# Optimization experiments

Measured on AMD Instinct MI355X. Metric: run time of the kernel, lower is better.

The kernel has to match this reference:

```python
import jax, jax.numpy as jnp
import numpy as np

FOCUS = 3.0
EPS = 1e-6


def setup_inputs() -> dict:
    key = jax.random.key(0)
    ks = jax.random.split(key, 8)
    C, h = 768, 12
    d = C // h
    H = W = T = 16
    l = 4
    Nx = H * W * T * l
    Nm = H * W * T
    B = 2

    def w(k, sh, s=0.02):
        return jax.random.normal(k, sh, jnp.float32) * s

    return {
        "x": jax.random.normal(ks[0], (Nx, B, C), jnp.float32),
        "memory": jax.random.normal(ks[1], (Nm, B, C), jnp.float32),
        "w_q": w(ks[2], (C, C)),
        "w_k": w(ks[3], (C, C)),
        "w_v": w(ks[4], (C, C)),
        "w_proj": w(ks[5], (C, C)),
        "b_proj": jnp.zeros((C,), jnp.float32),
        "dwc_w": w(ks[6], (d, 1, 5, 5)),
        "dwc_b": jnp.zeros((d,), jnp.float32),
        "scale": w(ks[7], (1, 1, C)),
        "H": H, "W": W, "T": T, "l": l,
    }


def _process(t, scale_sp):
    # focusing feature map: relu, rescale, elementwise power, renormalize to original norm
    t = jax.nn.relu(t) + EPS
    t = t / scale_sp
    n = jnp.linalg.norm(t, axis=-1, keepdims=True)
    tp = t ** FOCUS
    return tp / jnp.linalg.norm(tp, axis=-1, keepdims=True) * n


def _dwconv(v5, w, b):
    # depthwise conv2d, kernel 5, pad 2; v5: (B*h, d, H, W*T), w: (d,1,5,5)
    out = jax.lax.conv_general_dilated(
        v5, w, window_strides=(1, 1), padding=((2, 2), (2, 2)),
        dimension_numbers=("NCHW", "OIHW", "NCHW"),
        feature_group_count=v5.shape[1])
    return out + b[None, :, None, None]


def reference(x, memory, w_q, w_k, w_v, w_proj, b_proj, dwc_w, dwc_b, scale, H, W, T, l):
    x = x.transpose(1, 0, 2)          # (B, Nx, C)
    memory = memory.transpose(1, 0, 2)  # (B, Nm, C)
    B, Nx, C = x.shape
    Nm = memory.shape[1]
    d = dwc_w.shape[0]
    h = C // d

    q = jnp.einsum("bnc,dc->bnd", x, w_q)
    k = jnp.einsum("bnc,dc->bnd", memory, w_k)
    v = jnp.einsum("bnc,dc->bnd", memory, w_v)

    scale_sp = jax.nn.softplus(scale)
    q = _process(q, scale_sp)
    k = _process(k, scale_sp)

    q = q.reshape(B, Nx, h, d).transpose(0, 2, 1, 3)  # (B,h,Nx,d)
    k = k.reshape(B, Nm, h, d).transpose(0, 2, 1, 3)  # (B,h,Nm,d)
    v = v.reshape(B, Nm, h, d).transpose(0, 2, 1, 3)  # (B,h,Nm,d)

    k_mean = k.mean(axis=2, keepdims=True)            # (B,h,1,d)
    z = 1.0 / (jnp.einsum("bhnd,bhmd->bhnm", q, k_mean) + EPS)  # (B,h,Nx,1)

    inv = float(Nm) ** -0.5
    kv = jnp.einsum("bhnd,bhne->bhde", k * inv, v * inv)        # (B,h,d,d)
    out = jnp.einsum("bhnd,bhde->bhne", q, kv) * z              # (B,h,Nx,d)
    out = out.transpose(0, 2, 1, 3).reshape(B, Nx, C)

    # depthwise conv enhancement on v over (H, W*T) grid
    v5 = v.reshape(B * h, H, W, T, d).transpose(0, 4, 1, 2, 3).reshape(B * h, d, H, W * T)
    dwc = _dwconv(v5, dwc_w, dwc_b)                   # (B*h, d, H, W*T)
    dwc = dwc.reshape(B, C, Nm).transpose(0, 2, 1)    # (B, Nm, C)
    out = out + jnp.tile(dwc, (1, l, 1))              # (B, Nx, C)

    out = jnp.einsum("bnc,dc->bnd", out, w_proj) + b_proj
    return out.transpose(1, 0, 2)                     # (Nx, B, C)
```

## Files before the change

kernel.cpp:

```cpp
#include <hip/hip_runtime.h>

#define CD 768
#define NHEAD 12
#define DH 64
#define BSZ 2
#define NM_ 4096
#define NX_ 16384
#define EPSF 1e-6f
#define KSTR 1536
#define KVCH 32

using bf16x8 = __attribute__((ext_vector_type(8))) short;
using f32x4  = __attribute__((ext_vector_type(4))) float;

__device__ inline unsigned short bf16r(float f) {
  union { float f; unsigned u; } un; un.f = f;
  unsigned u = un.u;
  u += 0x7fffu + ((u >> 16) & 1u);
  return (unsigned short)(u >> 16);
}
__device__ inline float b2f(unsigned short u) {
  union { unsigned u; float f; } x; x.u = ((unsigned)u) << 16; return x.f;
}
__device__ inline float asf(unsigned u) {
  union { unsigned u; float f; } x; x.u = u; return x.f;
}
__device__ inline void gl2lds16(const void* g, void* l) {
  __builtin_amdgcn_global_load_lds(
      (const __attribute__((address_space(1))) void*)g,
      (__attribute__((address_space(3))) void*)l, 16, 0, 0);
}

__global__ __launch_bounds__(256) void prep_k(const float* __restrict__ w0, const float* __restrict__ w1,
                                              const float* __restrict__ w2, const float* __restrict__ w3,
                                              const float* __restrict__ scale,
                                              unsigned short* __restrict__ o0, unsigned short* __restrict__ o1,
                                              unsigned short* __restrict__ o2, unsigned short* __restrict__ o3,
                                              float* __restrict__ sp) {
  int bx = blockIdx.x;
  if (bx < 2304) {
    int m = bx / 576;
    int i = (bx % 576) * 256 + threadIdx.x;
    const float* w = m == 0 ? w0 : m == 1 ? w1 : m == 2 ? w2 : w3;
    unsigned short* o = m == 0 ? o0 : m == 1 ? o1 : m == 2 ? o2 : o3;
    float4 v = ((const float4*)w)[i];
    ushort4 u; u.x = bf16r(v.x); u.y = bf16r(v.y); u.z = bf16r(v.z); u.w = bf16r(v.w);
    ((ushort4*)o)[i] = u;
  } else {
    int i = (bx - 2304) * 256 + threadIdx.x;
    if (i < CD) sp[i] = log1pf(expf(scale[i]));
  }
}

__global__ __launch_bounds__(256) void cvt_k(const float* __restrict__ s,
                                             unsigned short* __restrict__ d, int n8) {
  int i = blockIdx.x * 256 + threadIdx.x;
  if (i >= n8) return;
  const float4* sp = (const float4*)s;
  float4 f0 = sp[(size_t)i * 2], f1 = sp[(size_t)i * 2 + 1];
  unsigned short u[8];
  u[0] = bf16r(f0.x); u[1] = bf16r(f0.y); u[2] = bf16r(f0.z); u[3] = bf16r(f0.w);
  u[4] = bf16r(f1.x); u[5] = bf16r(f1.y); u[6] = bf16r(f1.z); u[7] = bf16r(f1.w);
  *(int4*)(d + (size_t)i * 8) = *(int4*)u;
}

template<int OUTBF>
__global__ __launch_bounds__(256) void gemm128(const unsigned short* __restrict__ A,
                                               const unsigned short* __restrict__ B,
                                               void* __restrict__ Cv,
                                               const float* __restrict__ bias,
                                               int M, int N, int K) {
  __shared__ __align__(16) unsigned short As[128 * 32];
  __shared__ __align__(16) unsigned short Bs[128 * 32];
  const int m0 = blockIdx.x * 128, n0 = blockIdx.y * 128;
  const int tid = threadIdx.x, wave = tid >> 6, lane = tid & 63;
  const int quad = lane >> 4, l16 = lane & 15;
  const int wm = (wave >> 1) * 64, wn = (wave & 1) * 64;
  const int srow = lane >> 2, scol = (lane & 3) * 8;
  f32x4 acc[4][4] = {};
  for (int k0 = 0; k0 < K; k0 += 32) {
    __syncthreads();
    #pragma unroll
    for (int c2 = 0; c2 < 2; ++c2) {
      int ch = wave * 2 + c2;
      gl2lds16(A + (size_t)(m0 + ch * 16 + srow) * K + k0 + scol, (void*)(As + ch * 512));
      gl2lds16(B + (size_t)(n0 + ch * 16 + srow) * K + k0 + scol, (void*)(Bs + ch * 512));
    }
    __syncthreads();
    bf16x8 a[4], bb[4];
    #pragma unroll
    for (int t = 0; t < 4; ++t) {
      a[t]  = *(const bf16x8*)(As + (wm + t * 16 + l16) * 32 + quad * 8);
      bb[t] = *(const bf16x8*)(Bs + (wn + t * 16 + l16) * 32 + quad * 8);
    }
    #pragma unroll
    for (int tm = 0; tm < 4; ++tm)
      #pragma unroll
      for (int tn = 0; tn < 4; ++tn)
        acc[tm][tn] = __builtin_amdgcn_mfma_f32_16x16x32_bf16(a[tm], bb[tn], acc[tm][tn], 0, 0, 0);
  }
  #pragma unroll
  for (int tm = 0; tm < 4; ++tm)
    #pragma unroll
    for (int tn = 0; tn < 4; ++tn) {
      const int col = n0 + wn + tn * 16 + l16;
      const float bv = bias ? bias[col] : 0.f;
      #pragma unroll
      for (int r = 0; r < 4; ++r) {
        const int row = m0 + wm + tm * 16 + quad * 4 + r;
        float v = acc[tm][tn][r] + bv;
        if (OUTBF) ((unsigned short*)Cv)[(size_t)row * N + col] = bf16r(v);
        else       ((float*)Cv)[(size_t)row * N + col] = v;
      }
    }
}

template<int OUTBF>
__global__ __launch_bounds__(512, 2) void gemm256(const unsigned short* __restrict__ A,
                                                  const unsigned short* __restrict__ B,
                                                  void* __restrict__ Cv,
                                                  const float* __restrict__ bias,
                                                  int M, int N, int K) {
  __shared__ __align__(16) unsigned short As[4][256 * 32];
  __shared__ __align__(16) unsigned short Bs[4][256 * 32];
  const int m0 = blockIdx.x * 256, n0 = blockIdx.y * 256;
  const int tid = threadIdx.x, w = tid >> 6, lane = tid & 63;
  const int quad = lane >> 4, l16 = lane & 15;
  const int wm = (w >> 2) * 128, wn = (w & 3) * 64;
  const int NS = K >> 5;
  const int srow = 16 * w + (lane >> 2);
  const int c0 = lane & 3;
  const int scol = (c0 ^ ((srow >> 1) & 3)) * 8;
  const size_t arow = (size_t)(m0 + srow) * K;
  const size_t brow = (size_t)(n0 + srow) * K;
  const int fq = (quad ^ ((l16 >> 1) & 3)) * 8;

  auto stageA = [&](int s) {
    unsigned short* l = &As[s & 3][0] + w * 512;
    const size_t col = (size_t)s * 32 + scol;
    gl2lds16(A + arow + col, (void*)l);
    gl2lds16(A + arow + (size_t)128 * K + col, (void*)(l + 4096));
  };
  auto stageB = [&](int s) {
    unsigned short* l = &Bs[s & 3][0] + w * 512;
    const size_t col = (size_t)s * 32 + scol;
    gl2lds16(B + brow + col, (void*)l);
    gl2lds16(B + brow + (size_t)128 * K + col, (void*)(l + 4096));
  };

  f32x4 acc[8][4] = {};
  stageA(0); stageB(0);
  stageA(1); stageB(1);
  stageA(2); stageB(2);

  for (int s = 0; s < NS; ++s) {
    if (s < NS - 2)       asm volatile("s_waitcnt vmcnt(8)");
    else if (s == NS - 2) asm volatile("s_waitcnt vmcnt(4)");
    else                  asm volatile("s_waitcnt vmcnt(0)");
    __builtin_amdgcn_s_barrier();
    const unsigned short* sa = &As[s & 3][0];
    const unsigned short* sb = &Bs[s & 3][0];
    const bool st = (s + 3) < NS;
    bf16x8 av[4], bv[4];
    #pragma unroll
    for (int f = 0; f < 4; ++f) {
      av[f] = *(const bf16x8*)(sa + (wm + f * 16 + l16) * 32 + fq);
      bv[f] = *(const bf16x8*)(sb + (wn + f * 16 + l16) * 32 + fq);
    }
    if (st) stageA(s + 3);
    __builtin_amdgcn_s_setprio(1);
    #pragma unroll
    for (int mf = 0; mf < 4; ++mf)
      #pragma unroll
      for (int nf = 0; nf < 4; ++nf)
        acc[mf][nf] = __builtin_amdgcn_mfma_f32_16x16x32_bf16(av[mf], bv[nf], acc[mf][nf], 0, 0, 0);
    __builtin_amdgcn_s_setprio(0);
    __builtin_amdgcn_s_barrier();
    bf16x8 aw[4];
    #pragma unroll
    for (int f = 0; f < 4; ++f)
      aw[f] = *(const bf16x8*)(sa + (wm + 64 + f * 16 + l16) * 32 + fq);
    if (st) stageB(s + 3);
    __builtin_amdgcn_s_setprio(1);
    #pragma unroll
    for (int mf = 0; mf < 4; ++mf)
      #pragma unroll
      for (int nf = 0; nf < 4; ++nf)
        acc[4 + mf][nf] = __builtin_amdgcn_mfma_f32_16x16x32_bf16(aw[mf], bv[nf], acc[4 + mf][nf], 0, 0, 0);
    __builtin_amdgcn_s_setprio(0);
  }
  #pragma unroll
  for (int mf = 0; mf < 8; ++mf)
    #pragma unroll
    for (int nf = 0; nf < 4; ++nf) {
      const int col = n0 + wn + nf * 16 + l16;
      const float bvl = bias ? bias[col] : 0.f;
      #pragma unroll
      for (int r = 0; r < 4; ++r) {
        const int row = m0 + wm + mf * 16 + quad * 4 + r;
        float v = acc[mf][nf][r] + bvl;
        if (OUTBF) ((unsigned short*)Cv)[(size_t)row * N + col] = bf16r(v);
        else       ((float*)Cv)[(size_t)row * N + col] = v;
      }
    }
}

__global__ __launch_bounds__(256) void process_rows(float* __restrict__ X,
                                                    const float* __restrict__ sp) {
  const int row = blockIdx.x;
  const int tid = threadIdx.x;
  float* xr = X + (size_t)row * CD;
  float tv[3];
  float n2 = 0.f, m2 = 0.f;
  #pragma unroll
  for (int i = 0; i < 3; ++i) {
    int c = tid + i * 256;
    float t = fmaxf(xr[c], 0.f) + EPSF;
    t = t / sp[c];
    tv[i] = t;
    float t2 = t * t;
    n2 += t2;
    float p = t2 * t;
    m2 += p * p;
  }
  #pragma unroll
  for (int off = 32; off; off >>= 1) {
    n2 += __shfl_down(n2, off, 64);
    m2 += __shfl_down(m2, off, 64);
  }
  __shared__ float rn[4], rm[4];
  if ((tid & 63) == 0) { rn[tid >> 6] = n2; rm[tid >> 6] = m2; }
  __syncthreads();
  float N2 = rn[0] + rn[1] + rn[2] + rn[3];
  float M2 = rm[0] + rm[1] + rm[2] + rm[3];
  float factor = sqrtf(N2 / M2);
  unsigned short* xo = (unsigned short*)xr;
  #pragma unroll
  for (int i = 0; i < 3; ++i) {
    int c = tid + i * 256;
    float t = tv[i];
    xo[c] = bf16r(t * t * t * factor);
  }
}

__global__ __launch_bounds__(256) void kv_part_k(const unsigned short* __restrict__ Kp,
                                                 const unsigned short* __restrict__ Vp,
                                                 float* __restrict__ kvp,
                                                 float* __restrict__ kmp) {
  const int bh = blockIdx.x, chunk = blockIdx.y;
  const int b = bh / NHEAD, h = bh % NHEAD;
  const int n0 = chunk * 128;
  __shared__ __align__(16) unsigned short ks[128 * 72];
  __shared__ __align__(16) unsigned short vs[128 * 72];
  const int tid = threadIdx.x;
  #pragma unroll
  for (int it = 0; it < 4; ++it) {
    int g = it * 256 + tid;
    int row = g >> 3, c8 = (g & 7) * 8;
    int4 ka = *(const int4*)(Kp + ((size_t)(n0 + row) * BSZ + b) * KSTR + h * 64 + c8);
    int4 va = *(const int4*)(Vp + ((size_t)(n0 + row) * BSZ + b) * CD + h * 64 + c8);
    *(int4*)(ks + row * 72 + c8) = ka;
    *(int4*)(vs + row * 72 + c8) = va;
  }
  __syncthreads();
  const int d0 = (tid >> 4) * 4, e0 = (tid & 15) * 4;
  float acc[4][4] = {};
  #pragma unroll 4
  for (int n = 0; n < 128; ++n) {
    ushort4 kd = *(const ushort4*)(ks + n * 72 + d0);
    ushort4 ve = *(const ushort4*)(vs + n * 72 + e0);
    float kf[4] = {b2f(kd.x), b2f(kd.y), b2f(kd.z), b2f(kd.w)};
    float vf[4] = {b2f(ve.x), b2f(ve.y), b2f(ve.z), b2f(ve.w)};
    #pragma unroll
    for (int i = 0; i < 4; ++i)
      #pragma unroll
      for (int j = 0; j < 4; ++j) acc[i][j] += kf[i] * vf[j];
  }
  float* outp = kvp + ((size_t)chunk * 24 + bh) * 4096;
  #pragma unroll
  for (int i = 0; i < 4; ++i) {
    float4 o; o.x = acc[i][0]; o.y = acc[i][1]; o.z = acc[i][2]; o.w = acc[i][3];
    *(float4*)(outp + (d0 + i) * 64 + e0) = o;
  }
  if (tid < 64) {
    float s = 0.f;
    for (int n = 0; n < 128; ++n) s += b2f(ks[n * 72 + tid]);
    kmp[((size_t)chunk * 24 + bh) * 64 + tid] = s;
  }
}

__global__ __launch_bounds__(256) void kv_reduce_k(const float* __restrict__ kvp,
                                                   const float* __restrict__ kmp,
                                                   unsigned short* __restrict__ kvT,
                                                   float* __restrict__ km) {
  const int tid = threadIdx.x;
  const int bx = blockIdx.x;
  if (bx < 24) {
    __shared__ float t[64 * 65];
    float acc[16] = {};
    const float* base = kvp + (size_t)bx * 4096 + tid * 16;
    for (int c = 0; c < KVCH; ++c) {
      const float* p = base + (size_t)c * 24 * 4096;
      #pragma unroll
      for (int i = 0; i < 4; ++i) {
        float4 v = *(const float4*)(p + i * 4);
        acc[i * 4 + 0] += v.x; acc[i * 4 + 1] += v.y; acc[i * 4 + 2] += v.z; acc[i * 4 + 3] += v.w;
      }
    }
    const int d = tid >> 2, e0 = (tid & 3) * 16;
    #pragma unroll
    for (int i = 0; i < 16; ++i) t[d * 65 + e0 + i] = acc[i] * (1.f / NM_);
    __syncthreads();
    const int e = tid >> 2, dd0 = (tid & 3) * 16;
    ushort4 o[4];
    #pragma unroll
    for (int i = 0; i < 16; ++i)
      ((unsigned short*)o)[i] = bf16r(t[(dd0 + i) * 65 + e]);
    unsigned short* dst = kvT + (size_t)bx * 4096 + e * 64 + dd0;
    *(ushort4*)(dst) = o[0]; *(ushort4*)(dst + 4) = o[1];
    *(ushort4*)(dst + 8) = o[2]; *(ushort4*)(dst + 12) = o[3];
  } else {
    int i = (bx - 24) * 256 + tid;
    if (i < 24 * 64) {
      int bhh = i >> 6, d = i & 63;
      float s = 0.f;
      for (int c = 0; c < KVCH; ++c) s += kmp[((size_t)c * 24 + bhh) * 64 + d];
      int b = bhh / NHEAD, h = bhh % NHEAD;
      km[b * CD + h * 64 + d] = s * (1.f / NM_);
    }
  }
}

__global__ __launch_bounds__(256) void dwconv_k(const unsigned short* __restrict__ Vp,
                                                const float* __restrict__ w,
                                                const float* __restrict__ bias,
                                                unsigned short* __restrict__ outp) {
  __shared__ __align__(16) unsigned ls32[16 * 20 * 32];
  __shared__ float wsm[64 * 25];
  __shared__ float bsm[64];
  const int tid = threadIdx.x;
  const int bh = blockIdx.x, b = bh / NHEAD, h = bh % NHEAD;
  const int x0 = blockIdx.y * 16;
  for (int i = tid; i < 1600; i += 256) wsm[i] = w[i];
  if (tid < 64) bsm[tid] = bias[tid];
  const int lch = (tid & 7) * 8;
  #pragma unroll
  for (int it = 0; it < 10; ++it) {
    int p = it * 32 + (tid >> 3);
    int y = p / 20, xp = p % 20;
    int xx = x0 + xp - 2;
    int4 val = {0, 0, 0, 0};
    if (xx >= 0 && xx < 256)
      val = *(const int4*)(Vp + ((size_t)((y << 8) + xx) * BSZ + b) * CD + h * 64 + lch);
    *(int4*)((unsigned short*)ls32 + p * 64 + lch) = val;
  }
  __syncthreads();
  const int cp = tid & 31;
  const int xs = tid >> 5;
  float wr0[25], wr1[25];
  #pragma unroll
  for (int t = 0; t < 25; ++t) { wr0[t] = wsm[(cp * 2) * 25 + t]; wr1[t] = wsm[(cp * 2 + 1) * 25 + t]; }
  const float b0 = bsm[cp * 2], b1 = bsm[cp * 2 + 1];
  for (int y = 0; y < 16; ++y) {
    float a00 = b0, a01 = b1, a10 = b0, a11 = b1;
    #pragma unroll
    for (int dy = 0; dy < 5; ++dy) {
      int yy = y + dy - 2;
      if (yy < 0 || yy >= 16) continue;
      #pragma unroll
      for (int dx = 0; dx < 5; ++dx) {
        int base = (yy * 20 + xs * 2 + dx) * 32 + cp;
        unsigned u0 = ls32[base], u1 = ls32[base + 32];
        float w0 = wr0[dy * 5 + dx], w1 = wr1[dy * 5 + dx];
        a00 += w0 * asf(u0 << 16);  a01 += w1 * asf(u0 & 0xffff0000u);
        a10 += w0 * asf(u1 << 16);  a11 += w1 * asf(u1 & 0xffff0000u);
      }
    }
    const int x = x0 + xs * 2;
    size_t o = ((size_t)((y << 8) + x) * BSZ + b) * CD + h * 64 + cp * 2;
    ushort2 s0; s0.x = bf16r(a00); s0.y = bf16r(a01);
    ushort2 s1; s1.x = bf16r(a10); s1.y = bf16r(a11);
    *(ushort2*)(outp + o) = s0;
    *(ushort2*)(outp + o + (size_t)BSZ * CD) = s1;
  }
}

__global__ __launch_bounds__(256) void attn_mfma(const unsigned short* __restrict__ Qb,
                                                 const unsigned short* __restrict__ kvT,
                                                 const float* __restrict__ km,
                                                 const unsigned short* __restrict__ dwcb,
                                                 unsigned short* __restrict__ tmpb) {
  __shared__ __align__(16) unsigned short qs[128 * 64];
  __shared__ __align__(16) unsigned short kvs[64 * 64];
  __shared__ float kms[64];
  __shared__ float zs[128];
  const int bh = blockIdx.x, b = bh / NHEAD, h = bh % NHEAD;
  const int n0 = blockIdx.y * 128;
  const int tid = threadIdx.x, wave = tid >> 6, lane = tid & 63;
  const int quad = lane >> 4, l16 = lane & 15;
  #pragma unroll
  for (int c2 = 0; c2 < 4; ++c2) {
    int ch = wave * 4 + c2;
    int row = ch * 8 + (lane >> 3);
    int col = (lane & 7) * 8;
    gl2lds16(Qb + ((size_t)(n0 + row) * BSZ + b) * KSTR + h * 64 + col, (void*)(qs + ch * 512));
  }
  #pragma unroll
  for (int c2 = 0; c2 < 2; ++c2) {
    int ch = wave * 2 + c2;
    int e = ch * 8 + (lane >> 3);
    int col = (lane & 7) * 8;
    gl2lds16(kvT + (size_t)bh * 4096 + e * 64 + col, (void*)(kvs + ch * 512));
  }
  if (tid < 64) kms[tid] = km[b * CD + h * 64 + tid];
  __syncthreads();
  if (tid < 128) {
    float s = 0.f;
    for (int d2 = 0; d2 < 64; ++d2) s += b2f(qs[tid * 64 + d2]) * kms[d2];
    zs[tid] = 1.f / (s + EPSF);
  }
  __syncthreads();
  f32x4 acc[2][4] = {};
  #pragma unroll
  for (int kh = 0; kh < 2; ++kh) {
    bf16x8 a0 = *(const bf16x8*)(qs + (wave * 32 + l16) * 64 + kh * 32 + quad * 8);
    bf16x8 a1 = *(const bf16x8*)(qs + (wave * 32 + 16 + l16) * 64 + kh * 32 + quad * 8);
    bf16x8 bt[4];
    #pragma unroll
    for (int tn = 0; tn < 4; ++tn)
      bt[tn] = *(const bf16x8*)(kvs + (tn * 16 + l16) * 64 + kh * 32 + quad * 8);
    #pragma unroll
    for (int tn = 0; tn < 4; ++tn) {
      acc[0][tn] = __builtin_amdgcn_mfma_f32_16x16x32_bf16(a0, bt[tn], acc[0][tn], 0, 0, 0);
      acc[1][tn] = __builtin_amdgcn_mfma_f32_16x16x32_bf16(a1, bt[tn], acc[1][tn], 0, 0, 0);
    }
  }
  #pragma unroll
  for (int tm = 0; tm < 2; ++tm)
    #pragma unroll
    for (int tn = 0; tn < 4; ++tn)
      #pragma unroll
      for (int r = 0; r < 4; ++r) {
        int rl = wave * 32 + tm * 16 + quad * 4 + r;
        int n = n0 + rl;
        int m = n & (NM_ - 1);
        int c = h * 64 + tn * 16 + l16;
        float val = acc[tm][tn][r] * zs[rl] + b2f(dwcb[((size_t)m * BSZ + b) * CD + c]);
        tmpb[((size_t)n * BSZ + b) * CD + c] = bf16r(val);
      }
}

extern "C" void kernel_launch(void* const* d_in, const int* in_sizes, int n_in,
                              void* d_out, int out_size, void* d_ws, size_t ws_size,
                              hipStream_t stream) {
  const float* x      = (const float*)d_in[0];
  const float* memory = (const float*)d_in[1];
  const float* w_q    = (const float*)d_in[2];
  const float* w_k    = (const float*)d_in[3];
  const float* w_v    = (const float*)d_in[4];
  const float* w_proj = (const float*)d_in[5];
  const float* b_proj = (const float*)d_in[6];
  const float* dwc_w  = (const float*)d_in[7];
  const float* dwc_b  = (const float*)d_in[8];
  const float* scale  = (const float*)d_in[9];
  float* out = (float*)d_out;

  const int Mq = NX_ * BSZ;
  const int Mm = NM_ * BSZ;

  char* ws = (char*)d_ws;
  size_t off = 0;
  auto alloc = [&](size_t bytes) -> void* {
    void* p = ws + off;
    off += (bytes + 255) & ~(size_t)255;
    return p;
  };
  float* q    = (float*)alloc((size_t)Mq * CD * 4);
  float* kbuf = (float*)alloc((size_t)Mm * CD * 4);
  float* kvp  = (float*)alloc((size_t)KVCH * 24 * 4096 * 4);
  float* kmp  = (float*)alloc((size_t)KVCH * 24 * 64 * 4);
  float* km   = (float*)alloc((size_t)BSZ * CD * 4);
  float* sp   = (float*)alloc(CD * 4);
  unsigned short* tmpb = (unsigned short*)alloc((size_t)Mq * CD * 2);
  unsigned short* vb   = (unsigned short*)alloc((size_t)Mm * CD * 2);
  unsigned short* dwcb = (unsigned short*)alloc((size_t)Mm * CD * 2);
  unsigned short* kvT  = (unsigned short*)alloc((size_t)BSZ * NHEAD * DH * DH * 2);
  unsigned short* wqb  = (unsigned short*)alloc((size_t)CD * CD * 2);
  unsigned short* wkb  = (unsigned short*)alloc((size_t)CD * CD * 2);
  unsigned short* wvb  = (unsigned short*)alloc((size_t)CD * CD * 2);
  unsigned short* wpb  = (unsigned short*)alloc((size_t)CD * CD * 2);

  unsigned short* xb   = tmpb;
  unsigned short* memb = dwcb;

  prep_k<<<2307, 256, 0, stream>>>(w_q, w_k, w_v, w_proj, scale, wqb, wkb, wvb, wpb, sp);

  cvt_k<<<(Mq * CD / 8 + 255) / 256, 256, 0, stream>>>(x, xb, Mq * CD / 8);
  cvt_k<<<(Mm * CD / 8 + 255) / 256, 256, 0, stream>>>(memory, memb, Mm * CD / 8);

  gemm256<0><<<dim3(Mq / 256, CD / 256), 512, 0, stream>>>(xb,   wqb, q,    nullptr, Mq, CD, CD);
  gemm128<0><<<dim3(Mm / 128, CD / 128), 256, 0, stream>>>(memb, wkb, kbuf, nullptr, Mm, CD, CD);
  gemm128<1><<<dim3(Mm / 128, CD / 128), 256, 0, stream>>>(memb, wvb, vb,   nullptr, Mm, CD, CD);

  process_rows<<<Mq, 256, 0, stream>>>(q, sp);
  process_rows<<<Mm, 256, 0, stream>>>(kbuf, sp);

  const unsigned short* qb = (const unsigned short*)q;
  const unsigned short* kb = (const unsigned short*)kbuf;

  kv_part_k<<<dim3(24, KVCH), 256, 0, stream>>>(kb, vb, kvp, kmp);
  kv_reduce_k<<<30, 256, 0, stream>>>(kvp, kmp, kvT, km);

  dwconv_k<<<dim3(BSZ * NHEAD, 16), 256, 0, stream>>>(vb, dwc_w, dwc_b, dwcb);

  attn_mfma<<<dim3(BSZ * NHEAD, NX_ / 128), 256, 0, stream>>>(qb, kvT, km, dwcb, tmpb);

  gemm256<0><<<dim3(Mq / 256, CD / 256), 512, 0, stream>>>(tmpb, wpb, out, b_proj, Mq, CD, CD);
}
```

Measured before the change: 514.4 us.

## Replace 256x256 GEMM with 256x192-tile 1024-thread kernel using triple-buffered LDS

Replaces the 512-thread 256x256-tile GEMM used for the Q and output projections with a 1024-thread kernel using 256x192 tiles, giving a 128x4 grid instead of 128x3. Each of the 16 waves now owns a 64x48 sub-tile. The K loop is hardcoded to 768 and uses a three-buffer LDS ring, unrolled by three, with one barrier per step instead of two. The goal is more blocks and waves to fill the CUs and less synchronisation, at the cost of smaller per-wave tiles with lower MFMA reuse and a kernel that only works for K=768.

After: 510.5 us. About the same (-0.8%).

```diff
diff --git a/kernel.cpp b/kernel.cpp
--- a/kernel.cpp
+++ b/kernel.cpp
@@ -116,83 +116,72 @@
 }
 
 template<int OUTBF>
-__global__ __launch_bounds__(512, 2) void gemm256(const unsigned short* __restrict__ A,
-                                                  const unsigned short* __restrict__ B,
-                                                  void* __restrict__ Cv,
-                                                  const float* __restrict__ bias,
-                                                  int M, int N, int K) {
-  __shared__ __align__(16) unsigned short As[4][256 * 32];
-  __shared__ __align__(16) unsigned short Bs[4][256 * 32];
-  const int m0 = blockIdx.x * 256, n0 = blockIdx.y * 256;
+__global__ __launch_bounds__(1024, 4) void gemm256c(const unsigned short* __restrict__ A,
+                                                    const unsigned short* __restrict__ B,
+                                                    void* __restrict__ Cv,
+                                                    const float* __restrict__ bias,
+                                                    int M, int N) {
+  __shared__ __align__(16) unsigned short As0[8192], As1[8192], As2[8192];
+  __shared__ __align__(16) unsigned short Bs0[8192], Bs1[8192], Bs2[8192];
+  const int m0 = blockIdx.x * 256, n0 = blockIdx.y * 192;
   const int tid = threadIdx.x, w = tid >> 6, lane = tid & 63;
   const int quad = lane >> 4, l16 = lane & 15;
-  const int wm = (w >> 2) * 128, wn = (w & 3) * 64;
-  const int NS = K >> 5;
-  const int srow = 16 * w + (lane >> 2);
-  const int c0 = lane & 3;
-  const int scol = (c0 ^ ((srow >> 1) & 3)) * 8;
-  const size_t arow = (size_t)(m0 + srow) * K;
-  const size_t brow = (size_t)(n0 + srow) * K;
+  const int wm = (w >> 2) * 64, wn = (w & 3) * 48;
   const int fq = (quad ^ ((l16 >> 1) & 3)) * 8;
-
-  auto stageA = [&](int s) {
-    unsigned short* l = &As[s & 3][0] + w * 512;
-    const size_t col = (size_t)s * 32 + scol;
-    gl2lds16(A + arow + col, (void*)l);
-    gl2lds16(A + arow + (size_t)128 * K + col, (void*)(l + 4096));
+  const int lrow = lane >> 2, lc = lane & 3;
+  f32x4 acc[4][3] = {};
+
+  auto stage = [&](int s, unsigned short* la, unsigned short* lb) {
+    const int kc = s * 32;
+    #pragma unroll
+    for (int j = 0; j < 2; ++j) {
+      const int c = w * 2 + j;
+      if (c < 16) {
+        const int grow = c * 16 + lrow;
+        const int gcol = (lc ^ ((grow >> 1) & 3)) * 8;
+        gl2lds16(A + (size_t)(m0 + grow) * 768 + kc + gcol, (void*)(la + c * 512));
+      } else {
+        const int bc = (c < 28) ? c - 16 : c - 28;
+        const int grow = bc * 16 + lrow;
+        const int gcol = (lc ^ ((grow >> 1) & 3)) * 8;
+        gl2lds16(B + (size_t)(n0 + grow) * 768 + kc + gcol, (void*)(lb + (c - 16) * 512));
+      }
+    }
   };
-  auto stageB = [&](int s) {
-    unsigned short* l = &Bs[s & 3][0] + w * 512;
-    const size_t col = (size_t)s * 32 + scol;
-    gl2lds16(B + brow + col, (void*)l);
-    gl2lds16(B + brow + (size_t)128 * K + col, (void*)(l + 4096));
-  };
-
-  f32x4 acc[8][4] = {};
-  stageA(0); stageB(0);
-  stageA(1); stageB(1);
-  stageA(2); stageB(2);
-
-  for (int s = 0; s < NS; ++s) {
-    if (s < NS - 2)       asm volatile("s_waitcnt vmcnt(8)");
-    else if (s == NS - 2) asm volatile("s_waitcnt vmcnt(4)");
-    else                  asm volatile("s_waitcnt vmcnt(0)");
+
+  auto body = [&](int s, const unsigned short* sa, const unsigned short* sb,
+                  unsigned short* na, unsigned short* nb) {
+    if (s < 23) asm volatile("s_waitcnt vmcnt(2)");
+    else        asm volatile("s_waitcnt vmcnt(0)");
     __builtin_amdgcn_s_barrier();
-    const unsigned short* sa = &As[s & 3][0];
-    const unsigned short* sb = &Bs[s & 3][0];
-    const bool st = (s + 3) < NS;
-    bf16x8 av[4], bv[4];
-    #pragma unroll
-    for (int f = 0; f < 4; ++f) {
+    bf16x8 av[4], bv[3];
+    #pragma unroll
+    for (int f = 0; f < 4; ++f)
       av[f] = *(const bf16x8*)(sa + (wm + f * 16 + l16) * 32 + fq);
-      bv[f] = *(const bf16x8*)(sb + (wn + f * 16 + l16) * 32 + fq);
-    }
-    if (st) stageA(s + 3);
+    #pragma unroll
+    for (int nf = 0; nf < 3; ++nf)
+      bv[nf] = *(const bf16x8*)(sb + (wn + nf * 16 + l16) * 32 + fq);
+    if (s + 2 < 24) stage(s + 2, na, nb);
     __builtin_amdgcn_s_setprio(1);
     #pragma unroll
     for (int mf = 0; mf < 4; ++mf)
       #pragma unroll
-      for (int nf = 0; nf < 4; ++nf)
+      for (int nf = 0; nf < 3; ++nf)
         acc[mf][nf] = __builtin_amdgcn_mfma_f32_16x16x32_bf16(av[mf], bv[nf], acc[mf][nf], 0, 0, 0);
     __builtin_amdgcn_s_setprio(0);
-    __builtin_amdgcn_s_barrier();
-    bf16x8 aw[4];
-    #pragma unroll
-    for (int f = 0; f < 4; ++f)
-      aw[f] = *(const bf16x8*)(sa + (wm + 64 + f * 16 + l16) * 32 + fq);
-    if (st) stageB(s + 3);
-    __builtin_amdgcn_s_setprio(1);
-    #pragma unroll
-    for (int mf = 0; mf < 4; ++mf)
-      #pragma unroll
-      for (int nf = 0; nf < 4; ++nf)
-        acc[4 + mf][nf] = __builtin_amdgcn_mfma_f32_16x16x32_bf16(aw[mf], bv[nf], acc[4 + mf][nf], 0, 0, 0);
-    __builtin_amdgcn_s_setprio(0);
-  }
-  #pragma unroll
-  for (int mf = 0; mf < 8; ++mf)
-    #pragma unroll
-    for (int nf = 0; nf < 4; ++nf) {
+  };
+
+  stage(0, As0, Bs0);
+  stage(1, As1, Bs1);
+  for (int su = 0; su < 24; su += 3) {
+    body(su,     As0, Bs0, As2, Bs2);
+    body(su + 1, As1, Bs1, As0, Bs0);
+    body(su + 2, As2, Bs2, As1, Bs1);
+  }
+  #pragma unroll
+  for (int mf = 0; mf < 4; ++mf)
+    #pragma unroll
+    for (int nf = 0; nf < 3; ++nf) {
       const int col = n0 + wn + nf * 16 + l16;
       const float bvl = bias ? bias[col] : 0.f;
       #pragma unroll
@@ -498,7 +487,7 @@
   cvt_k<<<(Mq * CD / 8 + 255) / 256, 256, 0, stream>>>(x, xb, Mq * CD / 8);
   cvt_k<<<(Mm * CD / 8 + 255) / 256, 256, 0, stream>>>(memory, memb, Mm * CD / 8);
 
-  gemm256<0><<<dim3(Mq / 256, CD / 256), 512, 0, stream>>>(xb,   wqb, q,    nullptr, Mq, CD, CD);
+  gemm256c<0><<<dim3(Mq / 256, 4), 1024, 0, stream>>>(xb,   wqb, q,    nullptr, Mq, CD);
   gemm128<0><<<dim3(Mm / 128, CD / 128), 256, 0, stream>>>(memb, wkb, kbuf, nullptr, Mm, CD, CD);
   gemm128<1><<<dim3(Mm / 128, CD / 128), 256, 0, stream>>>(memb, wvb, vb,   nullptr, Mm, CD, CD);
 
@@ -515,5 +504,5 @@
 
   attn_mfma<<<dim3(BSZ * NHEAD, NX_ / 128), 256, 0, stream>>>(qb, kvT, km, dwcb, tmpb);
 
-  gemm256<0><<<dim3(Mq / 256, CD / 256), 512, 0, stream>>>(tmpb, wpb, out, b_proj, Mq, CD, CD);
-}
+  gemm256c<0><<<dim3(Mq / 256, 4), 1024, 0, stream>>>(tmpb, wpb, out, b_proj, Mq, CD);
+}
```

## Replace 4-stage gemm256 with double-buffered K=64 tile GEMM for Q/proj

Applied to the files above, without the earlier changes.

Replaces the 256x256 GEMM used for the Q projection and the output projection with a variant that hardcodes K=768 and uses 64-wide K tiles in two LDS buffers. Each half-tile is staged in four sub-steps interleaved with the MFMA phases, and it uses a different LDS swizzle. The aim is to cut barrier count per K element and to keep global-to-LDS loads overlapped with matrix math. In exchange the prefetch depth drops from three stages to one tile ahead, and the launch bounds no longer request two blocks per CU, which may lower occupancy.

Result: slower. 547.1 us (+6.3%).

```diff
diff --git a/kernel.cpp b/kernel.cpp
--- a/kernel.cpp
+++ b/kernel.cpp
@@ -116,78 +116,77 @@
 }
 
 template<int OUTBF>
-__global__ __launch_bounds__(512, 2) void gemm256(const unsigned short* __restrict__ A,
-                                                  const unsigned short* __restrict__ B,
-                                                  void* __restrict__ Cv,
-                                                  const float* __restrict__ bias,
-                                                  int M, int N, int K) {
-  __shared__ __align__(16) unsigned short As[4][256 * 32];
-  __shared__ __align__(16) unsigned short Bs[4][256 * 32];
+__global__ __launch_bounds__(512) void gemm8p(const unsigned short* __restrict__ A,
+                                              const unsigned short* __restrict__ B,
+                                              void* __restrict__ Cv,
+                                              const float* __restrict__ bias,
+                                              int M, int N) {
+  __shared__ __align__(16) unsigned short As[2 * 2 * 256 * 32];
+  __shared__ __align__(16) unsigned short Bs[2 * 2 * 256 * 32];
   const int m0 = blockIdx.x * 256, n0 = blockIdx.y * 256;
   const int tid = threadIdx.x, w = tid >> 6, lane = tid & 63;
   const int quad = lane >> 4, l16 = lane & 15;
   const int wm = (w >> 2) * 128, wn = (w & 3) * 64;
-  const int NS = K >> 5;
-  const int srow = 16 * w + (lane >> 2);
-  const int c0 = lane & 3;
-  const int scol = (c0 ^ ((srow >> 1) & 3)) * 8;
-  const size_t arow = (size_t)(m0 + srow) * K;
-  const size_t brow = (size_t)(n0 + srow) * K;
-  const int fq = (quad ^ ((l16 >> 1) & 3)) * 8;
-
-  auto stageA = [&](int s) {
-    unsigned short* l = &As[s & 3][0] + w * 512;
-    const size_t col = (size_t)s * 32 + scol;
-    gl2lds16(A + arow + col, (void*)l);
-    gl2lds16(A + arow + (size_t)128 * K + col, (void*)(l + 4096));
+  const int rswz = (quad ^ (l16 & 3)) * 8;
+  const int srow0 = (w * 2) * 16 + (lane >> 2);
+  const int scol  = ((lane & 3) ^ ((lane >> 2) & 3)) * 8;
+
+  auto stage_ht = [&](int Tn, int ht) {
+    const int kh = ht >> 1;
+    const int buf = Tn & 1;
+    const unsigned short* G = (ht & 1) ? B : A;
+    const int base = (ht & 1) ? n0 : m0;
+    unsigned short* L = ((ht & 1) ? Bs : As) + buf * 16384 + kh * 8192;
+    const int colg = Tn * 64 + kh * 32 + scol;
+    gl2lds16(G + (size_t)(base + srow0) * 768 + colg,      (void*)(L + (w * 2) * 512));
+    gl2lds16(G + (size_t)(base + srow0 + 16) * 768 + colg, (void*)(L + (w * 2 + 1) * 512));
   };
-  auto stageB = [&](int s) {
-    unsigned short* l = &Bs[s & 3][0] + w * 512;
-    const size_t col = (size_t)s * 32 + scol;
-    gl2lds16(B + brow + col, (void*)l);
-    gl2lds16(B + brow + (size_t)128 * K + col, (void*)(l + 4096));
-  };
 
   f32x4 acc[8][4] = {};
-  stageA(0); stageB(0);
-  stageA(1); stageB(1);
-  stageA(2); stageB(2);
-
-  for (int s = 0; s < NS; ++s) {
-    if (s < NS - 2)       asm volatile("s_waitcnt vmcnt(8)");
-    else if (s == NS - 2) asm volatile("s_waitcnt vmcnt(4)");
-    else                  asm volatile("s_waitcnt vmcnt(0)");
-    __builtin_amdgcn_s_barrier();
-    const unsigned short* sa = &As[s & 3][0];
-    const unsigned short* sb = &Bs[s & 3][0];
-    const bool st = (s + 3) < NS;
-    bf16x8 av[4], bv[4];
-    #pragma unroll
-    for (int f = 0; f < 4; ++f) {
-      av[f] = *(const bf16x8*)(sa + (wm + f * 16 + l16) * 32 + fq);
-      bv[f] = *(const bf16x8*)(sb + (wn + f * 16 + l16) * 32 + fq);
-    }
-    if (st) stageA(s + 3);
-    __builtin_amdgcn_s_setprio(1);
-    #pragma unroll
-    for (int mf = 0; mf < 4; ++mf)
+  stage_ht(0, 0); stage_ht(0, 1); stage_ht(0, 2); stage_ht(0, 3);
+
+  for (int T = 0; T < 12; ++T) {
+    const int buf = T & 1;
+    const unsigned short* ab = As + buf * 16384;
+    const unsigned short* bb = Bs + buf * 16384;
+    #pragma unroll
+    for (int kh = 0; kh < 2; ++kh) {
+      const unsigned short* abk = ab + kh * 8192;
+      const unsigned short* bbk = bb + kh * 8192;
+      if (T < 11 || kh == 0) asm volatile("s_waitcnt vmcnt(4)");
+      else                   asm volatile("s_waitcnt vmcnt(0)");
+      __builtin_amdgcn_s_barrier();
+      __builtin_amdgcn_sched_barrier(0);
+      bf16x8 av[4], bv[4];
       #pragma unroll
       for (int nf = 0; nf < 4; ++nf)
-        acc[mf][nf] = __builtin_amdgcn_mfma_f32_16x16x32_bf16(av[mf], bv[nf], acc[mf][nf], 0, 0, 0);
-    __builtin_amdgcn_s_setprio(0);
-    __builtin_amdgcn_s_barrier();
-    bf16x8 aw[4];
-    #pragma unroll
-    for (int f = 0; f < 4; ++f)
-      aw[f] = *(const bf16x8*)(sa + (wm + 64 + f * 16 + l16) * 32 + fq);
-    if (st) stageB(s + 3);
-    __builtin_amdgcn_s_setprio(1);
-    #pragma unroll
-    for (int mf = 0; mf < 4; ++mf)
-      #pragma unroll
-      for (int nf = 0; nf < 4; ++nf)
-        acc[4 + mf][nf] = __builtin_amdgcn_mfma_f32_16x16x32_bf16(aw[mf], bv[nf], acc[4 + mf][nf], 0, 0, 0);
-    __builtin_amdgcn_s_setprio(0);
+        bv[nf] = *(const bf16x8*)(bbk + (wn + nf * 16 + l16) * 32 + rswz);
+      #pragma unroll
+      for (int f = 0; f < 4; ++f)
+        av[f] = *(const bf16x8*)(abk + (wm + f * 16 + l16) * 32 + rswz);
+      if (T < 11) stage_ht(T + 1, kh * 2);
+      __builtin_amdgcn_s_setprio(1);
+      #pragma unroll
+      for (int mf = 0; mf < 4; ++mf)
+        #pragma unroll
+        for (int nf = 0; nf < 4; ++nf)
+          acc[mf][nf] = __builtin_amdgcn_mfma_f32_16x16x32_bf16(av[mf], bv[nf], acc[mf][nf], 0, 0, 0);
+      __builtin_amdgcn_s_setprio(0);
+      __builtin_amdgcn_s_barrier();
+      bf16x8 aw[4];
+      #pragma unroll
+      for (int f = 0; f < 4; ++f)
+        aw[f] = *(const bf16x8*)(abk + (wm + 64 + f * 16 + l16) * 32 + rswz);
+      if (T < 11) stage_ht(T + 1, kh * 2 + 1);
+      __builtin_amdgcn_s_setprio(1);
+      #pragma unroll
+      for (int mf = 0; mf < 4; ++mf)
+        #pragma unroll
+        for (int nf = 0; nf < 4; ++nf)
+          acc[4 + mf][nf] = __builtin_amdgcn_mfma_f32_16x16x32_bf16(aw[mf], bv[nf], acc[4 + mf][nf], 0, 0, 0);
+      __builtin_amdgcn_s_setprio(0);
+      __builtin_amdgcn_s_barrier();
+    }
   }
   #pragma unroll
   for (int mf = 0; mf < 8; ++mf)
@@ -498,7 +497,7 @@
   cvt_k<<<(Mq * CD / 8 + 255) / 256, 256, 0, stream>>>(x, xb, Mq * CD / 8);
   cvt_k<<<(Mm * CD / 8 + 255) / 256, 256, 0, stream>>>(memory, memb, Mm * CD / 8);
 
-  gemm256<0><<<dim3(Mq / 256, CD / 256), 512, 0, stream>>>(xb,   wqb, q,    nullptr, Mq, CD, CD);
+  gemm8p<0><<<dim3(Mq / 256, CD / 256), 512, 0, stream>>>(xb, wqb, q, nullptr, Mq, CD);
   gemm128<0><<<dim3(Mm / 128, CD / 128), 256, 0, stream>>>(memb, wkb, kbuf, nullptr, Mm, CD, CD);
   gemm128<1><<<dim3(Mm / 128, CD / 128), 256, 0, stream>>>(memb, wvb, vb,   nullptr, Mm, CD, CD);
 
@@ -515,5 +514,5 @@
 
   attn_mfma<<<dim3(BSZ * NHEAD, NX_ / 128), 256, 0, stream>>>(qb, kvT, km, dwcb, tmpb);
 
-  gemm256<0><<<dim3(Mq / 256, CD / 256), 512, 0, stream>>>(tmpb, wpb, out, b_proj, Mq, CD, CD);
-}
+  gemm8p<0><<<dim3(Mq / 256, CD / 256), 512, 0, stream>>>(tmpb, wpb, out, b_proj, Mq, CD);
+}
```
